# Kernel tuning notes

Measured on AMD Instinct MI355X. Metric: run time of the kernel, lower is better.

The kernel has to match this reference:

```python
import jax, jax.numpy as jnp
import numpy as np

N_NODES = 100000
N_EDGES = 3200000
F_IN = 128
F_OUT = 16


def setup_inputs() -> dict:
    key = jax.random.key(0)
    k1, k2, k3, k4, k5 = jax.random.split(key, 5)
    x = jax.random.normal(k1, (N_NODES, F_IN), dtype=jnp.float32)
    edge_index = jax.random.randint(k2, (2, N_EDGES), 0, N_NODES, dtype=jnp.int64)
    edge_weights = jax.random.uniform(k3, (N_EDGES,), dtype=jnp.float32)
    W = jax.random.normal(k4, (F_IN, F_OUT), dtype=jnp.float32) / np.sqrt(F_IN)
    b = jax.random.normal(k5, (F_OUT,), dtype=jnp.float32)
    return {"x": x, "edge_index": edge_index, "edge_weights": edge_weights, "W": W, "b": b}


def reference(x, edge_index, edge_weights, W, b):
    # GCNConv: out = D^{-1/2} (A + I) D^{-1/2} X W + b  (weighted edges, self-loops)
    n = x.shape[0]
    row = edge_index[0]  # source nodes
    col = edge_index[1]  # target nodes (aggregation destination)
    # add self-loops with weight 1.0 (GCNConv default)
    loop = jnp.arange(n, dtype=row.dtype)
    row_f = jnp.concatenate([row, loop])
    col_f = jnp.concatenate([col, loop])
    ew = jnp.concatenate([edge_weights, jnp.ones((n,), dtype=edge_weights.dtype)])
    # symmetric normalization: deg over destination, norm = d^{-1/2}[row] * w * d^{-1/2}[col]
    deg = jax.ops.segment_sum(ew, col_f, num_segments=n)
    dinv = jnp.where(deg > 0, jax.lax.rsqrt(deg), 0.0)
    norm = dinv[row_f] * ew * dinv[col_f]  # [E+N]
    h = x @ W  # [N, F_OUT] dense projection before propagation
    msgs = h[row_f] * norm[:, None]  # gather + scale, [E+N, F_OUT]
    out = jax.ops.segment_sum(msgs, col_f, num_segments=n)  # scatter-add
    return out + b
```

## Files before the change

### kernel.cpp

```cpp
#include <hip/hip_runtime.h>

#define N_NODES 100000
#define N_EDGES 3200000
#define F_IN 128
#define F_OUT 16

#define NSEG 512
#define EPS (N_EDGES / NSEG)
#define NBUCK 512
#define NPB 196
#define CAPR 7424
#define GEMM_BLOCKS ((N_NODES + 15) / 16)
#define PULL_BLOCKS 2048

#define OFF_CUR   0x000000u
#define OFF_NPTR  0x010000u
#define OFF_NCNT  0x080000u
#define OFF_DINV  0x0F0000u
#define OFF_HH    0x160000u
#define OFF_GG    0x780000u
#define OFF_CSR   0xB00000u
#define WS_NEEDED ((size_t)0x1000000 + (size_t)N_EDGES * 8)

__device__ __forceinline__ unsigned short f2bf(float f) {
    unsigned u = __float_as_uint(f);
    unsigned r = (u + 0x7FFFu + ((u >> 16) & 1u)) >> 16;
    return (unsigned short)r;
}
__device__ __forceinline__ float bf2f(unsigned short v) {
    return __uint_as_float((unsigned)v << 16);
}


__global__ void k_gemm(const float* __restrict__ x, const float* __restrict__ W,
                       float* __restrict__ h, int* __restrict__ cursor) {
    int tid = threadIdx.x;
    if (blockIdx.x == GEMM_BLOCKS) {
        cursor[tid] = tid * CAPR;
        cursor[tid + 256] = (tid + 256) * CAPR;
        return;
    }
    __shared__ float Ws[F_IN * F_OUT];
    for (int i = tid; i < F_IN * F_OUT; i += 256) Ws[i] = W[i];
    __syncthreads();
    int n = blockIdx.x * 16 + (tid >> 4);
    int j = tid & 15;
    if (n >= N_NODES) return;
    const float4* xr = (const float4*)(x + (size_t)n * F_IN);
    float acc = 0.0f;
#pragma unroll
    for (int k4 = 0; k4 < F_IN / 4; ++k4) {
        float4 xv = xr[k4];
        int k = k4 * 4;
        acc += xv.x * Ws[(k + 0) * F_OUT + j];
        acc += xv.y * Ws[(k + 1) * F_OUT + j];
        acc += xv.z * Ws[(k + 2) * F_OUT + j];
        acc += xv.w * Ws[(k + 3) * F_OUT + j];
    }
    h[(size_t)n * F_OUT + j] = acc;
}

__global__ void __launch_bounds__(512) k_bin2(const int* __restrict__ row,
                                              const int* __restrict__ col,
                                              const float* __restrict__ ew,
                                              int* __restrict__ cursor,
                                              int2* __restrict__ csr) {
    __shared__ int2 srec[EPS];
    __shared__ unsigned char sbk[EPS];
    __shared__ int lcnt[NBUCK];
    __shared__ int lpre[NBUCK];
    __shared__ int gofs[NBUCK];
    __shared__ int wtot[8];
    int tid = threadIdx.x;
    int e0 = blockIdx.x * EPS;

    lcnt[tid] = 0;
    __syncthreads();
    for (int i = tid; i < EPS; i += 512)
        atomicAdd(&lcnt[col[e0 + i] / NPB], 1);
    __syncthreads();

    int v = lcnt[tid];
    int inc = v;
#pragma unroll
    for (int off = 1; off < 64; off <<= 1) {
        int t = __shfl_up(inc, off);
        if ((tid & 63) >= off) inc += t;
    }
    if ((tid & 63) == 63) wtot[tid >> 6] = inc;
    __syncthreads();
    int woff = 0;
#pragma unroll
    for (int k = 0; k < 8; ++k)
        if (k < (tid >> 6)) woff += wtot[k];
    int excl = woff + inc - v;
    lpre[tid] = excl;
    int gstart = atomicAdd(&cursor[tid], v);
    gofs[tid] = gstart - excl;
    lcnt[tid] = excl;
    __syncthreads();

    for (int i = tid; i < EPS; i += 512) {
        int e = e0 + i;
        int r = row[e];
        int c = col[e];
        int bk = c / NPB;
        int pos = atomicAdd(&lcnt[bk], 1);
        srec[pos] = make_int2((r << 8) | (c - bk * NPB), __float_as_int(ew[e]));
        sbk[pos] = (unsigned char)bk;
    }
    __syncthreads();

    int mid = lpre[256];
    for (int t = tid; t < EPS; t += 512) {
        int bk = sbk[t] + ((t >= mid) ? 256 : 0);
        csr[gofs[bk] + t] = srec[t];
    }
}

__global__ void __launch_bounds__(256) k_sort2(const int* __restrict__ cursor,
                                               int2* __restrict__ csr,
                                               const float* __restrict__ h,
                                               float* __restrict__ dinv,
                                               unsigned short* __restrict__ gb,
                                               int* __restrict__ nodeptr,
                                               int* __restrict__ ncnt) {
    __shared__ int2 srec[CAPR];
    __shared__ int cnt[256];
    __shared__ int cur[256];
    __shared__ int wtot[4];
    float* dl = (float*)cnt;
    int tid = threadIdx.x;
    int b = blockIdx.x;
    int c0 = b * NPB;
    int rb = b * CAPR;
    int total = cursor[b] - rb;
    if (total > CAPR) total = CAPR;

    cnt[tid] = 0;
    __syncthreads();
    for (int i = tid; i < total; i += 256) {
        int2 rec = csr[rb + i];
        srec[i] = rec;
        atomicAdd(&cnt[rec.x & 255], 1);
    }
    __syncthreads();

    int v = cnt[tid];
    int inc = v;
#pragma unroll
    for (int off = 1; off < 64; off <<= 1) {
        int t = __shfl_up(inc, off);
        if ((tid & 63) >= off) inc += t;
    }
    if ((tid & 63) == 63) wtot[tid >> 6] = inc;
    __syncthreads();
    int woff = 0;
#pragma unroll
    for (int k = 0; k < 4; ++k)
        if (k < (tid >> 6)) woff += wtot[k];
    int excl = woff + inc - v;
    int n = c0 + tid;
    if (tid < NPB && n < N_NODES) {
        nodeptr[n] = rb + excl;
        ncnt[n] = v;
    }
    cur[tid] = excl;
    __syncthreads();

    for (int i = tid; i < total; i += 256) {
        int2 rec = srec[i];
        int pos = atomicAdd(&cur[rec.x & 255], 1);
        csr[rb + pos] = make_int2(rec.x >> 8, rec.y);
    }
    __syncthreads();

    float d = 0.0f;
    if (tid < NPB && n < N_NODES) {
        float s = 1.0f;
        const int2* run = csr + rb + excl;
        for (int k = 0; k < v; ++k) s += __int_as_float(run[k].y);
        d = rsqrtf(s);
        dinv[n] = d;
    }
    __syncthreads();
    dl[tid] = d;
    __syncthreads();
    for (int i = tid; i < NPB * F_OUT; i += 256) {
        int idx = c0 * F_OUT + i;
        if (idx < N_NODES * F_OUT) gb[idx] = f2bf(dl[i >> 4] * h[idx]);
    }
}

__global__ void __launch_bounds__(256) k_pull4(const int* __restrict__ nodeptr,
                                               const int* __restrict__ ncnt,
                                               const int2* __restrict__ csr,
                                               const unsigned short* __restrict__ gb,
                                               const float* __restrict__ dinv,
                                               const float* __restrict__ bias,
                                               float* __restrict__ out) {
    int wid = threadIdx.x >> 6;
    int lane = threadIdx.x & 63;
    int l4 = lane & 15;
    int fr = ((l4 & 1) << 3) | ((l4 & 2) << 1) | ((l4 & 4) >> 1) | ((l4 & 8) >> 3);
    float bj = bias[fr];
    for (int n = blockIdx.x * 4 + wid; n < N_NODES; n += PULL_BLOCKS * 4) {
        int p0 = nodeptr[n];
        int c = ncnt[n];
        float acc[16];
#pragma unroll
        for (int k = 0; k < 16; ++k) acc[k] = 0.0f;
        for (int base = 0; base < c; base += 64) {
            int i = base + lane;
            int2 rec = (i < c) ? csr[p0 + i] : make_int2(0, 0);
            float w = __int_as_float(rec.y);
            const uint4* gr = (const uint4*)(gb + ((size_t)rec.x << 4));
            uint4 qa = gr[0];
            uint4 qb = gr[1];
            acc[0]  += w * __uint_as_float(qa.x << 16);
            acc[1]  += w * __uint_as_float(qa.x & 0xFFFF0000u);
            acc[2]  += w * __uint_as_float(qa.y << 16);
            acc[3]  += w * __uint_as_float(qa.y & 0xFFFF0000u);
            acc[4]  += w * __uint_as_float(qa.z << 16);
            acc[5]  += w * __uint_as_float(qa.z & 0xFFFF0000u);
            acc[6]  += w * __uint_as_float(qa.w << 16);
            acc[7]  += w * __uint_as_float(qa.w & 0xFFFF0000u);
            acc[8]  += w * __uint_as_float(qb.x << 16);
            acc[9]  += w * __uint_as_float(qb.x & 0xFFFF0000u);
            acc[10] += w * __uint_as_float(qb.y << 16);
            acc[11] += w * __uint_as_float(qb.y & 0xFFFF0000u);
            acc[12] += w * __uint_as_float(qb.z << 16);
            acc[13] += w * __uint_as_float(qb.z & 0xFFFF0000u);
            acc[14] += w * __uint_as_float(qb.w << 16);
            acc[15] += w * __uint_as_float(qb.w & 0xFFFF0000u);
        }
        bool b1 = (lane & 1) != 0;
#pragma unroll
        for (int k = 0; k < 8; ++k) {
            float keep = b1 ? acc[k + 8] : acc[k];
            float send = b1 ? acc[k] : acc[k + 8];
            acc[k] = keep + __shfl_xor(send, 1);
        }
        bool b2 = (lane & 2) != 0;
#pragma unroll
        for (int k = 0; k < 4; ++k) {
            float keep = b2 ? acc[k + 4] : acc[k];
            float send = b2 ? acc[k] : acc[k + 4];
            acc[k] = keep + __shfl_xor(send, 2);
        }
        bool b4 = (lane & 4) != 0;
#pragma unroll
        for (int k = 0; k < 2; ++k) {
            float keep = b4 ? acc[k + 2] : acc[k];
            float send = b4 ? acc[k] : acc[k + 2];
            acc[k] = keep + __shfl_xor(send, 4);
        }
        bool b8 = (lane & 8) != 0;
        {
            float keep = b8 ? acc[1] : acc[0];
            float send = b8 ? acc[0] : acc[1];
            acc[0] = keep + __shfl_xor(send, 8);
        }
        acc[0] += __shfl_xor(acc[0], 16);
        acc[0] += __shfl_xor(acc[0], 32);
        if (lane < 16) {
            float d = dinv[n];
            float gs = bf2f(gb[(size_t)n * F_OUT + fr]);
            out[(size_t)n * F_OUT + fr] = bj + d * (gs + acc[0]);
        }
    }
}


#define EDGE_BLOCKS_FB ((N_EDGES + 255) / 256)
__global__ void k_init_fb(float* __restrict__ deg) {
    int i = blockIdx.x * blockDim.x + threadIdx.x;
    if (i < N_NODES) deg[i] = 1.0f;
}
__global__ void k_fused_fb(const int* __restrict__ col, const float* __restrict__ ew,
                           float* __restrict__ deg, const float* __restrict__ x,
                           const float* __restrict__ W, float* __restrict__ h) {
    int b3 = blockIdx.x / 3;
    int r3 = blockIdx.x % 3;
    if (r3 < 2) {
        int e = (b3 * 2 + r3) * 256 + threadIdx.x;
        if (e < N_EDGES) atomicAdd(&deg[col[e]], ew[e]);
    } else {
        __shared__ float Ws[F_IN * F_OUT];
        int tid = threadIdx.x;
        for (int i = tid; i < F_IN * F_OUT; i += 256) Ws[i] = W[i];
        __syncthreads();
        int n = b3 * 16 + (tid >> 4);
        int j = tid & 15;
        if (n >= N_NODES) return;
        const float4* xr = (const float4*)(x + (size_t)n * F_IN);
        float acc = 0.0f;
#pragma unroll
        for (int k4 = 0; k4 < F_IN / 4; ++k4) {
            float4 xv = xr[k4];
            int k = k4 * 4;
            acc += xv.x * Ws[(k + 0) * F_OUT + j];
            acc += xv.y * Ws[(k + 1) * F_OUT + j];
            acc += xv.z * Ws[(k + 2) * F_OUT + j];
            acc += xv.w * Ws[(k + 3) * F_OUT + j];
        }
        h[(size_t)n * F_OUT + j] = acc;
    }
}
__global__ void k_final_fb(float* __restrict__ deg, const float* __restrict__ h,
                           const float* __restrict__ b, float* __restrict__ g,
                           float* __restrict__ out) {
    int i = blockIdx.x * blockDim.x + threadIdx.x;
    int n = i >> 4;
    int j = i & 15;
    if (n >= N_NODES) return;
    float d = rsqrtf(deg[n]);
    if (j == 0) deg[n] = d;
    float gg = d * h[i];
    g[i] = gg;
    out[i] = b[j] + d * gg;
}
__global__ void k_scatter_fb(const int* __restrict__ row, const int* __restrict__ col,
                             const float* __restrict__ ew, const float* __restrict__ dinv,
                             const float* __restrict__ g, float* __restrict__ out) {
    long long tid = (long long)blockIdx.x * blockDim.x + threadIdx.x;
    int e = (int)(tid >> 4);
    int j = (int)(tid & 15);
    if (e >= N_EDGES) return;
    int c = col[e];
    float norm = ew[e] * dinv[c];
    atomicAdd(&out[(size_t)c * F_OUT + j], g[(size_t)row[e] * F_OUT + j] * norm);
}

extern "C" void kernel_launch(void* const* d_in, const int* in_sizes, int n_in,
                              void* d_out, int out_size, void* d_ws, size_t ws_size,
                              hipStream_t stream) {
    const float* x  = (const float*)d_in[0];
    const int*   ei = (const int*)d_in[1];
    const float* ew = (const float*)d_in[2];
    const float* W  = (const float*)d_in[3];
    const float* b  = (const float*)d_in[4];
    float* out = (float*)d_out;

    const int* row = ei;
    const int* col = ei + N_EDGES;

    char* ws = (char*)d_ws;
    dim3 blk(256);

    if (ws_size >= WS_NEEDED) {
        int*   cur  = (int*)(ws + OFF_CUR);
        int*   nptr = (int*)(ws + OFF_NPTR);
        int*   ncnt = (int*)(ws + OFF_NCNT);
        float* dinv = (float*)(ws + OFF_DINV);
        float* h    = (float*)(ws + OFF_HH);
        unsigned short* gb = (unsigned short*)(ws + OFF_GG);
        int2*  csr  = (int2*)(ws + OFF_CSR);

        k_gemm<<<GEMM_BLOCKS + 1, blk, 0, stream>>>(x, W, h, cur);
        k_bin2<<<NSEG, 512, 0, stream>>>(row, col, ew, cur, csr);
        k_sort2<<<NBUCK, blk, 0, stream>>>(cur, csr, h, dinv, gb, nptr, ncnt);
        k_pull4<<<PULL_BLOCKS, blk, 0, stream>>>(nptr, ncnt, csr, gb, dinv, b, out);
    } else {
        float* deg = (float*)ws;
        float* h   = (float*)(ws + (1u << 20));
        float* g   = (float*)(ws + (8u << 20));
        k_init_fb<<<(N_NODES + 255) / 256, blk, 0, stream>>>(deg);
        k_fused_fb<<<EDGE_BLOCKS_FB + GEMM_BLOCKS, blk, 0, stream>>>(col, ew, deg, x, W, h);
        k_final_fb<<<(N_NODES * F_OUT + 255) / 256, blk, 0, stream>>>(deg, h, b, g, out);
        long long total = (long long)N_EDGES * F_OUT;
        k_scatter_fb<<<(unsigned)((total + 255) / 256), blk, 0, stream>>>(row, col, ew, deg, g, out);
    }
}
```

Measured before the change: 247.1 us.

## Fuse GEMM into binning kernel and make binning single-pass with register-held records

The dense projection moves into the binning kernel as extra blocks, which removes a separate launch and lets the GEMM overlap with edge binning. Binning now reads each edge once, keeps records in registers with their local slot (from a shared atomic), and scatters them straight to the bucket's region. This drops the two-pass count, the block prefix scan and the large shared staging. Cursor initialisation becomes a memset with relative offsets. The sort kernel records each record's atomic slot during counting, so the second atomic pass is gone, and one barrier is removed. In exchange, the scatter order inside a bucket is no longer grouped by bucket, so global writes are less coalesced.

```diff
diff --git a/kernel.cpp b/kernel.cpp
--- a/kernel.cpp
+++ b/kernel.cpp
@@ -7,10 +7,11 @@
 
 #define NSEG 512
 #define EPS (N_EDGES / NSEG)
+#define EPT 13
 #define NBUCK 512
 #define NPB 196
 #define CAPR 7424
-#define GEMM_BLOCKS ((N_NODES + 15) / 16)
+#define GEMM32 ((N_NODES + 31) / 32)
 #define PULL_BLOCKS 2048
 
 #define OFF_CUR   0x000000u
@@ -32,93 +33,76 @@
 }
 
 
-__global__ void k_gemm(const float* __restrict__ x, const float* __restrict__ W,
-                       float* __restrict__ h, int* __restrict__ cursor) {
-    int tid = threadIdx.x;
-    if (blockIdx.x == GEMM_BLOCKS) {
-        cursor[tid] = tid * CAPR;
-        cursor[tid + 256] = (tid + 256) * CAPR;
-        return;
-    }
-    __shared__ float Ws[F_IN * F_OUT];
-    for (int i = tid; i < F_IN * F_OUT; i += 256) Ws[i] = W[i];
-    __syncthreads();
-    int n = blockIdx.x * 16 + (tid >> 4);
-    int j = tid & 15;
-    if (n >= N_NODES) return;
-    const float4* xr = (const float4*)(x + (size_t)n * F_IN);
-    float acc = 0.0f;
-#pragma unroll
-    for (int k4 = 0; k4 < F_IN / 4; ++k4) {
-        float4 xv = xr[k4];
-        int k = k4 * 4;
-        acc += xv.x * Ws[(k + 0) * F_OUT + j];
-        acc += xv.y * Ws[(k + 1) * F_OUT + j];
-        acc += xv.z * Ws[(k + 2) * F_OUT + j];
-        acc += xv.w * Ws[(k + 3) * F_OUT + j];
-    }
-    h[(size_t)n * F_OUT + j] = acc;
-}
-
-__global__ void __launch_bounds__(512) k_bin2(const int* __restrict__ row,
+__global__ void __launch_bounds__(512) k_binA(const int* __restrict__ row,
                                               const int* __restrict__ col,
                                               const float* __restrict__ ew,
                                               int* __restrict__ cursor,
-                                              int2* __restrict__ csr) {
-    __shared__ int2 srec[EPS];
-    __shared__ unsigned char sbk[EPS];
-    __shared__ int lcnt[NBUCK];
-    __shared__ int lpre[NBUCK];
-    __shared__ int gofs[NBUCK];
-    __shared__ int wtot[8];
+                                              int2* __restrict__ csr,
+                                              const float* __restrict__ x,
+                                              const float* __restrict__ W,
+                                              float* __restrict__ h) {
+    __shared__ int smem[2048];
     int tid = threadIdx.x;
-    int e0 = blockIdx.x * EPS;
-
-    lcnt[tid] = 0;
-    __syncthreads();
-    for (int i = tid; i < EPS; i += 512)
-        atomicAdd(&lcnt[col[e0 + i] / NPB], 1);
-    __syncthreads();
-
-    int v = lcnt[tid];
-    int inc = v;
-#pragma unroll
-    for (int off = 1; off < 64; off <<= 1) {
-        int t = __shfl_up(inc, off);
-        if ((tid & 63) >= off) inc += t;
-    }
-    if ((tid & 63) == 63) wtot[tid >> 6] = inc;
-    __syncthreads();
-    int woff = 0;
-#pragma unroll
-    for (int k = 0; k < 8; ++k)
-        if (k < (tid >> 6)) woff += wtot[k];
-    int excl = woff + inc - v;
-    lpre[tid] = excl;
-    int gstart = atomicAdd(&cursor[tid], v);
-    gofs[tid] = gstart - excl;
-    lcnt[tid] = excl;
-    __syncthreads();
-
-    for (int i = tid; i < EPS; i += 512) {
-        int e = e0 + i;
-        int r = row[e];
-        int c = col[e];
-        int bk = c / NPB;
-        int pos = atomicAdd(&lcnt[bk], 1);
-        srec[pos] = make_int2((r << 8) | (c - bk * NPB), __float_as_int(ew[e]));
-        sbk[pos] = (unsigned char)bk;
-    }
-    __syncthreads();
-
-    int mid = lpre[256];
-    for (int t = tid; t < EPS; t += 512) {
-        int bk = sbk[t] + ((t >= mid) ? 256 : 0);
-        csr[gofs[bk] + t] = srec[t];
-    }
-}
-
-__global__ void __launch_bounds__(256) k_sort2(const int* __restrict__ cursor,
+    if (blockIdx.x < NSEG) {
+        int* lcnt = smem;
+        int* gofs = smem + 512;
+        int e0 = blockIdx.x * EPS;
+        lcnt[tid] = 0;
+        __syncthreads();
+
+        int2 rec[EPT];
+        int meta[EPT];
+#pragma unroll
+        for (int k = 0; k < EPT; ++k) {
+            int i = k * 512 + tid;
+            if (k < EPT - 1 || i < EPS) {
+                int e = e0 + i;
+                int r = row[e];
+                int c = col[e];
+                float w = ew[e];
+                int bk = c / NPB;
+                int pos = atomicAdd(&lcnt[bk], 1);
+                rec[k] = make_int2((r << 8) | (c - bk * NPB), __float_as_int(w));
+                meta[k] = (bk << 16) | pos;
+            }
+        }
+        __syncthreads();
+
+        int v = lcnt[tid];
+        gofs[tid] = tid * CAPR + atomicAdd(&cursor[tid], v);
+        __syncthreads();
+
+#pragma unroll
+        for (int k = 0; k < EPT; ++k) {
+            int i = k * 512 + tid;
+            if (k < EPT - 1 || i < EPS) {
+                int m = meta[k];
+                csr[gofs[m >> 16] + (m & 0xFFFF)] = rec[k];
+            }
+        }
+    } else {
+        float* Ws = (float*)smem;
+        for (int i = tid; i < F_IN * F_OUT; i += 512) Ws[i] = W[i];
+        __syncthreads();
+        int n = (blockIdx.x - NSEG) * 32 + (tid >> 4);
+        int j = tid & 15;
+        if (n >= N_NODES) return;
+        const float4* xr = (const float4*)(x + (size_t)n * F_IN);
+        float acc = 0.0f;
+#pragma unroll
+        for (int k4 = 0; k4 < F_IN / 4; ++k4) {
+            float4 xv = xr[k4];
+            int k = k4 * 4;
+            acc += xv.x * Ws[(k + 0) * F_OUT + j];
+            acc += xv.y * Ws[(k + 1) * F_OUT + j];
+            acc += xv.z * Ws[(k + 2) * F_OUT + j];
+            acc += xv.w * Ws[(k + 3) * F_OUT + j];
+        }
+        h[(size_t)n * F_OUT + j] = acc;
+    }
+}
+
+__global__ void __launch_bounds__(256) k_sortA(const int* __restrict__ cursor,
                                                int2* __restrict__ csr,
                                                const float* __restrict__ h,
                                                float* __restrict__ dinv,
@@ -126,15 +110,16 @@
                                                int* __restrict__ nodeptr,
                                                int* __restrict__ ncnt) {
     __shared__ int2 srec[CAPR];
+    __shared__ unsigned short spos[CAPR];
     __shared__ int cnt[256];
-    __shared__ int cur[256];
+    __shared__ int basel[256];
     __shared__ int wtot[4];
-    float* dl = (float*)cnt;
+    __shared__ float dl[256];
     int tid = threadIdx.x;
     int b = blockIdx.x;
     int c0 = b * NPB;
     int rb = b * CAPR;
-    int total = cursor[b] - rb;
+    int total = cursor[b];
     if (total > CAPR) total = CAPR;
 
     cnt[tid] = 0;
@@ -142,7 +127,7 @@
     for (int i = tid; i < total; i += 256) {
         int2 rec = csr[rb + i];
         srec[i] = rec;
-        atomicAdd(&cnt[rec.x & 255], 1);
+        spos[i] = (unsigned short)atomicAdd(&cnt[rec.x & 255], 1);
     }
     __syncthreads();
 
@@ -165,13 +150,13 @@
         nodeptr[n] = rb + excl;
         ncnt[n] = v;
     }
-    cur[tid] = excl;
+    basel[tid] = excl;
     __syncthreads();
 
     for (int i = tid; i < total; i += 256) {
         int2 rec = srec[i];
-        int pos = atomicAdd(&cur[rec.x & 255], 1);
-        csr[rb + pos] = make_int2(rec.x >> 8, rec.y);
+        int p = basel[rec.x & 255] + spos[i];
+        csr[rb + p] = make_int2(rec.x >> 8, rec.y);
     }
     __syncthreads();
 
@@ -183,7 +168,6 @@
         d = rsqrtf(s);
         dinv[n] = d;
     }
-    __syncthreads();
     dl[tid] = d;
     __syncthreads();
     for (int i = tid; i < NPB * F_OUT; i += 256) {
@@ -273,6 +257,7 @@
 
 
 #define EDGE_BLOCKS_FB ((N_EDGES + 255) / 256)
+#define GEMM_BLOCKS_FB ((N_NODES + 15) / 16)
 __global__ void k_init_fb(float* __restrict__ deg) {
     int i = blockIdx.x * blockDim.x + threadIdx.x;
     if (i < N_NODES) deg[i] = 1.0f;
@@ -357,16 +342,16 @@
         unsigned short* gb = (unsigned short*)(ws + OFF_GG);
         int2*  csr  = (int2*)(ws + OFF_CSR);
 
-        k_gemm<<<GEMM_BLOCKS + 1, blk, 0, stream>>>(x, W, h, cur);
-        k_bin2<<<NSEG, 512, 0, stream>>>(row, col, ew, cur, csr);
-        k_sort2<<<NBUCK, blk, 0, stream>>>(cur, csr, h, dinv, gb, nptr, ncnt);
+        hipMemsetAsync(cur, 0, NBUCK * sizeof(int), stream);
+        k_binA<<<NSEG + GEMM32, 512, 0, stream>>>(row, col, ew, cur, csr, x, W, h);
+        k_sortA<<<NBUCK, blk, 0, stream>>>(cur, csr, h, dinv, gb, nptr, ncnt);
         k_pull4<<<PULL_BLOCKS, blk, 0, stream>>>(nptr, ncnt, csr, gb, dinv, b, out);
     } else {
         float* deg = (float*)ws;
         float* h   = (float*)(ws + (1u << 20));
         float* g   = (float*)(ws + (8u << 20));
         k_init_fb<<<(N_NODES + 255) / 256, blk, 0, stream>>>(deg);
-        k_fused_fb<<<EDGE_BLOCKS_FB + GEMM_BLOCKS, blk, 0, stream>>>(col, ew, deg, x, W, h);
+        k_fused_fb<<<EDGE_BLOCKS_FB + GEMM_BLOCKS_FB, blk, 0, stream>>>(col, ew, deg, x, W, h);
         k_final_fb<<<(N_NODES * F_OUT + 255) / 256, blk, 0, stream>>>(deg, h, b, g, out);
         long long total = (long long)N_EDGES * F_OUT;
         k_scatter_fb<<<(unsigned)((total + 255) / 256), blk, 0, stream>>>(row, col, ew, deg, g, out);
```

Result: faster. 239.4 us (-3.1%).
